# Performance work log

Hardware: AMD Instinct MI355X
Metric: run time of the kernel (lower is better)

The kernel has to match this reference:

```python
import jax, jax.numpy as jnp
import numpy as np

DEPTH_CHANNELS = 64
OUT_CHANNELS = 128
IN_CHANNELS = 256
BEV_W, BEV_H = 432, 496  # interpolate target size (height=432, width=496 in torch's (H,W) order)


def setup_inputs() -> dict:
    key = jax.random.key(0)
    k1, k2 = jax.random.split(key)
    B, H, W = 4, 32, 88
    feat_2d = jax.random.normal(k1, (B, IN_CHANNELS, H, W), dtype=jnp.float32)
    # conv1x1 weight: (out=64+128, in=256), bias (192,)
    Wc = jax.random.normal(k2, (DEPTH_CHANNELS + OUT_CHANNELS, IN_CHANNELS), dtype=jnp.float32) * 0.02
    bc = jnp.zeros((DEPTH_CHANNELS + OUT_CHANNELS,), dtype=jnp.float32)
    return {"feat_2d": feat_2d, "Wc": Wc, "bc": bc}


def reference(feat_2d, Wc, bc):
    # 1x1 conv == channel GEMM
    x = jnp.einsum('bihw,oi->bohw', feat_2d, Wc) + bc[None, :, None, None]
    depth = jax.nn.softmax(x[:, :DEPTH_CHANNELS], axis=1)      # (B,64,H,W)
    context = x[:, DEPTH_CHANNELS:]                            # (B,C,H,W)
    # mean_d(context[c] * depth[d]) == context[c] * mean_d(depth)  (algebraically identical)
    bev = context * jnp.mean(depth, axis=1, keepdims=True)     # (B,C,H,W)
    # bilinear upsample, half-pixel convention == torch align_corners=False (upsampling)
    B, C = bev.shape[0], bev.shape[1]
    bev = jax.image.resize(bev, (B, C, BEV_W, BEV_H), method='bilinear')
    return bev
```

## Files before the change

### kernel.cpp

```cpp
#include <hip/hip_runtime.h>


#define K_IN    256
#define C_CTX   128
#define C_DEPTH 64
#define H_IN    32
#define W_IN    88
#define POS     (H_IN * W_IN)
#define H_OUT   432
#define W_OUT   496
#define XG      (W_OUT / 4)
#define GPP     (XG * H_OUT)
#define NPLANE  (4 * C_CTX)

__global__ __launch_bounds__(256) void conv1x1_kernel(
    const float* __restrict__ feat, const float* __restrict__ Wc,
    const float* __restrict__ bc, float* __restrict__ ctx)
{
    int p4 = blockIdx.x * blockDim.x + threadIdx.x;
    if (p4 >= POS / 4) return;
    const int c0 = blockIdx.y * 4;
    const int b  = blockIdx.z;

    const float* fb = feat + (size_t)b * K_IN * POS + 4 * p4;
    const float* w  = Wc + (size_t)(C_DEPTH + c0) * K_IN;

    float4 a0 = {0.f, 0.f, 0.f, 0.f};
    float4 a1 = {0.f, 0.f, 0.f, 0.f};
    float4 a2 = {0.f, 0.f, 0.f, 0.f};
    float4 a3 = {0.f, 0.f, 0.f, 0.f};

    #pragma unroll 8
    for (int i = 0; i < K_IN; ++i) {
        float4 f = *(const float4*)(fb + (size_t)i * POS);
        float w0 = w[i];
        float w1 = w[K_IN + i];
        float w2 = w[2 * K_IN + i];
        float w3 = w[3 * K_IN + i];
        a0.x = fmaf(f.x, w0, a0.x); a0.y = fmaf(f.y, w0, a0.y);
        a0.z = fmaf(f.z, w0, a0.z); a0.w = fmaf(f.w, w0, a0.w);
        a1.x = fmaf(f.x, w1, a1.x); a1.y = fmaf(f.y, w1, a1.y);
        a1.z = fmaf(f.z, w1, a1.z); a1.w = fmaf(f.w, w1, a1.w);
        a2.x = fmaf(f.x, w2, a2.x); a2.y = fmaf(f.y, w2, a2.y);
        a2.z = fmaf(f.z, w2, a2.z); a2.w = fmaf(f.w, w2, a2.w);
        a3.x = fmaf(f.x, w3, a3.x); a3.y = fmaf(f.y, w3, a3.y);
        a3.z = fmaf(f.z, w3, a3.z); a3.w = fmaf(f.w, w3, a3.w);
    }

    const float s = 1.0f / 64.0f;
    float4 accs[4] = {a0, a1, a2, a3};
    #pragma unroll
    for (int j = 0; j < 4; ++j) {
        float bb = bc[C_DEPTH + c0 + j];
        float4 r;
        r.x = (accs[j].x + bb) * s;
        r.y = (accs[j].y + bb) * s;
        r.z = (accs[j].z + bb) * s;
        r.w = (accs[j].w + bb) * s;
        *(float4*)(ctx + ((size_t)(b * C_CTX + c0 + j) * POS + 4 * p4)) = r;
    }
}

__global__ __launch_bounds__(256) void resize_kernel(
    const float* __restrict__ ctx, float* __restrict__ out)
{
    int g = blockIdx.x * blockDim.x + threadIdx.x;
    if (g >= GPP) return;
    int y  = g / XG;
    int xg = g - y * XG;
    int plane = blockIdx.y;

    const float* p = ctx + (size_t)plane * POS;

    const float SCY = 32.0f / 432.0f;
    const float SCX = 88.0f / 496.0f;

    float sy = (y + 0.5f) * SCY - 0.5f;
    float fyf = floorf(sy);
    float wy = sy - fyf;
    int y0 = (int)fyf;
    int y0c = max(y0, 0);
    int y1c = min(y0 + 1, H_IN - 1);
    const float* r0 = p + y0c * W_IN;
    const float* r1 = p + y1c * W_IN;

    float sx0 = (4 * xg + 0.5f) * SCX - 0.5f;
    int xb = (int)floorf(sx0);

    float ry[3];
    #pragma unroll
    for (int t = 0; t < 3; ++t) {
        int xt = min(max(xb + t, 0), W_IN - 1);
        float a = r0[xt];
        float b = r1[xt];
        ry[t] = a + wy * (b - a);
    }

    float o[4];
    #pragma unroll
    for (int j = 0; j < 4; ++j) {
        float s  = (4 * xg + j + 0.5f) * SCX - 0.5f;
        float fs = floorf(s);
        float fx = s - fs;
        int t = (int)fs - xb;
        o[j] = ry[t] + fx * (ry[t + 1] - ry[t]);
    }

    size_t oidx = ((size_t)plane * H_OUT + y) * W_OUT + 4 * xg;
    float4 v = {o[0], o[1], o[2], o[3]};
    *(float4*)(out + oidx) = v;
}

extern "C" void kernel_launch(void* const* d_in, const int* in_sizes, int n_in,
                              void* d_out, int out_size, void* d_ws, size_t ws_size,
                              hipStream_t stream) {
    const float* feat = (const float*)d_in[0];
    const float* Wc   = (const float*)d_in[1];
    const float* bc   = (const float*)d_in[2];
    float* out = (float*)d_out;
    float* ctx = (float*)d_ws;

    dim3 b1(256);
    dim3 g1((POS / 4 + 255) / 256, C_CTX / 4, 4);
    conv1x1_kernel<<<g1, b1, 0, stream>>>(feat, Wc, bc, ctx);

    dim3 b2(256);
    dim3 g2((GPP + 255) / 256, NPLANE);
    resize_kernel<<<g2, b2, 0, stream>>>(ctx, out);
}
```

Baseline: 476.0 us.

## Tile conv1x1 GEMM through LDS with register prefetch and wave-uniform weights

```diff
diff --git a/kernel.cpp b/kernel.cpp
--- a/kernel.cpp
+++ b/kernel.cpp
@@ -13,51 +13,79 @@
 #define GPP     (XG * H_OUT)
 #define NPLANE  (4 * C_CTX)
 
+#define KC      64
+#define BPOS    64
+#define LROW    68
+
 __global__ __launch_bounds__(256) void conv1x1_kernel(
     const float* __restrict__ feat, const float* __restrict__ Wc,
     const float* __restrict__ bc, float* __restrict__ ctx)
 {
-    int p4 = blockIdx.x * blockDim.x + threadIdx.x;
-    if (p4 >= POS / 4) return;
-    const int c0 = blockIdx.y * 4;
-    const int b  = blockIdx.z;
+    __shared__ float fs[BPOS * LROW];
 
-    const float* fb = feat + (size_t)b * K_IN * POS + 4 * p4;
-    const float* w  = Wc + (size_t)(C_DEPTH + c0) * K_IN;
+    const int t       = threadIdx.x;
+    const int posbase = blockIdx.x * BPOS;
+    const int b       = blockIdx.z;
+    const int wave    = __builtin_amdgcn_readfirstlane(t >> 6);
+    const int cbase   = blockIdx.y * 64 + wave * 16;
+    const int lane    = t & 63;
 
-    float4 a0 = {0.f, 0.f, 0.f, 0.f};
-    float4 a1 = {0.f, 0.f, 0.f, 0.f};
-    float4 a2 = {0.f, 0.f, 0.f, 0.f};
-    float4 a3 = {0.f, 0.f, 0.f, 0.f};
+    const float* fb  = feat + (size_t)b * K_IN * POS + posbase;
+    const int kl0 = t >> 4;
+    const int p0  = (t & 15) * 4;
 
-    #pragma unroll 8
-    for (int i = 0; i < K_IN; ++i) {
-        float4 f = *(const float4*)(fb + (size_t)i * POS);
-        float w0 = w[i];
-        float w1 = w[K_IN + i];
-        float w2 = w[2 * K_IN + i];
-        float w3 = w[3 * K_IN + i];
-        a0.x = fmaf(f.x, w0, a0.x); a0.y = fmaf(f.y, w0, a0.y);
-        a0.z = fmaf(f.z, w0, a0.z); a0.w = fmaf(f.w, w0, a0.w);
-        a1.x = fmaf(f.x, w1, a1.x); a1.y = fmaf(f.y, w1, a1.y);
-        a1.z = fmaf(f.z, w1, a1.z); a1.w = fmaf(f.w, w1, a1.w);
-        a2.x = fmaf(f.x, w2, a2.x); a2.y = fmaf(f.y, w2, a2.y);
-        a2.z = fmaf(f.z, w2, a2.z); a2.w = fmaf(f.w, w2, a2.w);
-        a3.x = fmaf(f.x, w3, a3.x); a3.y = fmaf(f.y, w3, a3.y);
-        a3.z = fmaf(f.z, w3, a3.z); a3.w = fmaf(f.w, w3, a3.w);
+    float4 pre[4];
+    #pragma unroll
+    for (int j = 0; j < 4; ++j)
+        pre[j] = *(const float4*)(fb + (size_t)(kl0 + 16 * j) * POS + p0);
+
+    float acc[16];
+    #pragma unroll
+    for (int c = 0; c < 16; ++c) acc[c] = 0.f;
+
+    const float* wbase = Wc + (size_t)(C_DEPTH + cbase) * K_IN;
+
+    for (int kc = 0; kc < K_IN / KC; ++kc) {
+        #pragma unroll
+        for (int j = 0; j < 4; ++j) {
+            int kl = kl0 + 16 * j;
+            fs[(p0 + 0) * LROW + kl] = pre[j].x;
+            fs[(p0 + 1) * LROW + kl] = pre[j].y;
+            fs[(p0 + 2) * LROW + kl] = pre[j].z;
+            fs[(p0 + 3) * LROW + kl] = pre[j].w;
+        }
+        __syncthreads();
+
+        if (kc + 1 < K_IN / KC) {
+            const float* fn = fb + (size_t)(kc + 1) * KC * POS;
+            #pragma unroll
+            for (int j = 0; j < 4; ++j)
+                pre[j] = *(const float4*)(fn + (size_t)(kl0 + 16 * j) * POS + p0);
+        }
+
+        const float* wk = wbase + kc * KC;
+        #pragma unroll
+        for (int kk = 0; kk < KC; kk += 4) {
+            float4 f = *(const float4*)&fs[lane * LROW + kk];
+            #pragma unroll
+            for (int c = 0; c < 16; ++c) {
+                const float* w4 = wk + c * K_IN + kk;
+                float a = acc[c];
+                a = fmaf(f.x, w4[0], a);
+                a = fmaf(f.y, w4[1], a);
+                a = fmaf(f.z, w4[2], a);
+                a = fmaf(f.w, w4[3], a);
+                acc[c] = a;
+            }
+        }
+        __syncthreads();
     }
 
     const float s = 1.0f / 64.0f;
-    float4 accs[4] = {a0, a1, a2, a3};
     #pragma unroll
-    for (int j = 0; j < 4; ++j) {
-        float bb = bc[C_DEPTH + c0 + j];
-        float4 r;
-        r.x = (accs[j].x + bb) * s;
-        r.y = (accs[j].y + bb) * s;
-        r.z = (accs[j].z + bb) * s;
-        r.w = (accs[j].w + bb) * s;
-        *(float4*)(ctx + ((size_t)(b * C_CTX + c0 + j) * POS + 4 * p4)) = r;
+    for (int c = 0; c < 16; ++c) {
+        float v = (acc[c] + bc[C_DEPTH + cbase + c]) * s;
+        ctx[(size_t)(b * C_CTX + cbase + c) * POS + posbase + lane] = v;
     }
 }
 
@@ -75,10 +103,10 @@
     const float SCY = 32.0f / 432.0f;
     const float SCX = 88.0f / 496.0f;
 
-    float sy = (y + 0.5f) * SCY - 0.5f;
+    float sy  = (y + 0.5f) * SCY - 0.5f;
     float fyf = floorf(sy);
-    float wy = sy - fyf;
-    int y0 = (int)fyf;
+    float wy  = sy - fyf;
+    int y0  = (int)fyf;
     int y0c = max(y0, 0);
     int y1c = min(y0 + 1, H_IN - 1);
     const float* r0 = p + y0c * W_IN;
@@ -89,11 +117,11 @@
 
     float ry[3];
     #pragma unroll
-    for (int t = 0; t < 3; ++t) {
-        int xt = min(max(xb + t, 0), W_IN - 1);
+    for (int tp = 0; tp < 3; ++tp) {
+        int xt = min(max(xb + tp, 0), W_IN - 1);
         float a = r0[xt];
         float b = r1[xt];
-        ry[t] = a + wy * (b - a);
+        ry[tp] = a + wy * (b - a);
     }
 
     float o[4];
@@ -102,8 +130,8 @@
         float s  = (4 * xg + j + 0.5f) * SCX - 0.5f;
         float fs = floorf(s);
         float fx = s - fs;
-        int t = (int)fs - xb;
-        o[j] = ry[t] + fx * (ry[t + 1] - ry[t]);
+        int tp = (int)fs - xb;
+        o[j] = ry[tp] + fx * (ry[tp + 1] - ry[tp]);
     }
 
     size_t oidx = ((size_t)plane * H_OUT + y) * W_OUT + 4 * xg;
@@ -121,7 +149,7 @@
     float* ctx = (float*)d_ws;
 
     dim3 b1(256);
-    dim3 g1((POS / 4 + 255) / 256, C_CTX / 4, 4);
+    dim3 g1(POS / BPOS, C_CTX / 64, 4);
     conv1x1_kernel<<<g1, b1, 0, stream>>>(feat, Wc, bc, ctx);
 
     dim3 b2(256);
```

After: 503.4 us. 1.06x slower.
